# Kernel tuning notes

Hardware: AMD Instinct MI355X
Metric: run time of the kernel (lower is better)

Reference implementation:

```python
import jax, jax.numpy as jnp
import numpy as np

B, N, H, D = 1024, 128, 128, 8  # batch, num_nodes (= num variables), hidden, diffusion size


def setup_inputs() -> dict:
    key = jax.random.key(0)
    ks = jax.random.split(key, 7)
    return {
        "x": jax.random.normal(ks[0], (B, N), dtype=jnp.float32),
        "f_weight": jax.random.normal(ks[1], (N, N, H), dtype=jnp.float32) * 0.1,
        "g_weight": jax.random.normal(ks[2], (N, N, H, D), dtype=jnp.float32) * 0.1,
        "Wf": jax.random.normal(ks[3], (N, H), dtype=jnp.float32) * (1.0 / np.sqrt(H)),
        "bf": jax.random.normal(ks[4], (N,), dtype=jnp.float32) * 0.01,
        "Wg": jax.random.normal(ks[5], (N, H), dtype=jnp.float32) * (1.0 / np.sqrt(H)),
        "bg": jax.random.normal(ks[6], (N,), dtype=jnp.float32) * 0.01,
    }


def reference(x, f_weight, g_weight, Wf, bf, Wg, bg):
    # Drift f: per node i, temp_i = x @ f_weight[i]  -> [B,H]; out_i = fc_i(elu(temp_i)) -> [B,1]
    # Batched over nodes as a single einsum instead of the original Python loop.
    temp_f = jnp.einsum('bn,inh->bih', x, f_weight)              # [B,N,H]
    f_out = jnp.einsum('bih,ih->bi', jax.nn.elu(temp_f), Wf) + bf  # [B,N]

    # Diffusion g: per node i, temp_i = x @ g_weight[i] -> [B,H,D]; fc_i applied over H per diffusion channel.
    temp_g = jnp.einsum('bn,inhd->bihd', x, g_weight)            # [B,N,H,D]
    g_out = jnp.einsum('bihd,ih->bid', jax.nn.elu(temp_g), Wg) + bg[None, :, None]  # [B,N,D]
    return f_out, g_out
```

## Files before the change

kernel.cpp:

```cpp
#include <hip/hip_runtime.h>
#include <hip/hip_bf16.h>


typedef unsigned short u16;
typedef __attribute__((ext_vector_type(8))) short bf16x8;
typedef __attribute__((ext_vector_type(4))) float f32x4;

#define LOG2E 1.4426950408889634f
#define LN2   0.6931471805599453f

__device__ __forceinline__ uint32_t pk2(float a, float b) {
    union { __hip_bfloat162 h2; uint32_t u; } c;
    c.h2 = __float22bfloat162_rn(make_float2(a, b));
    return c.u;
}
__device__ __forceinline__ float elu_acc(float u, float wv, float p) {
    float m = fmaxf(u, 0.f);
    float e = __builtin_amdgcn_exp2f(fminf(u, 0.f));
    return fmaf(fmaf(m, LN2, e), wv, p);
}

__global__ __launch_bounds__(512, 2) void sde_fused(
    const float* __restrict__ x, const float* __restrict__ fw, const float* __restrict__ gw,
    const float* __restrict__ Wf, const float* __restrict__ bfp,
    const float* __restrict__ Wg, const float* __restrict__ bgp,
    float* __restrict__ out)
{
    __shared__ u16 wst[2][64 * 128];
    __shared__ float wgs[128];
    __shared__ float wfs[128];

    const int t = threadIdx.x, bx = blockIdx.x;
    const int i    = bx & 127;
    const int b0   = (bx >> 7) << 9;
    const int w    = t >> 6;
    const int lane = t & 63;
    const int l15  = lane & 15;
    const int quad = lane >> 4;
    const int l31  = lane & 31;
    const int jj   = lane >> 5;
    const int c0   = l31 * 2;
    const int sw   = (l15 >> 1) & 7;
    const int j    = w * 2 + jj;

    if (t < 128) { wgs[t] = Wg[i * 128 + t]; wfs[t] = Wf[i * 128 + t]; }

    const float* gwi = gw + (size_t)i * 131072;
    const float* fwi = fw + (size_t)i * 16384;

    float2 vr[8];
    auto load_tile = [&](int ct) {
        const float* src; int rstride;
        if (ct < 16) { src = gwi + ct * 64;        rstride = 1024; }
        else         { src = fwi + (ct - 16) * 64; rstride = 128;  }
        const float* s2 = src + (size_t)(8 * j) * rstride + c0;
        #pragma unroll
        for (int r = 0; r < 8; ++r) vr[r] = *(const float2*)(s2 + (size_t)r * rstride);
    };
    auto write_tile = [&](int p) {
        const int slot = (j ^ (l31 & 7)) << 3;
        union { uint32_t u[4]; bf16x8 v; } rr;
        rr.u[0] = pk2(vr[0].x, vr[1].x); rr.u[1] = pk2(vr[2].x, vr[3].x);
        rr.u[2] = pk2(vr[4].x, vr[5].x); rr.u[3] = pk2(vr[6].x, vr[7].x);
        *(bf16x8*)&wst[p][c0 * 128 + slot] = rr.v;
        rr.u[0] = pk2(vr[0].y, vr[1].y); rr.u[1] = pk2(vr[2].y, vr[3].y);
        rr.u[2] = pk2(vr[4].y, vr[5].y); rr.u[3] = pk2(vr[6].y, vr[7].y);
        *(bf16x8*)&wst[p][(c0 + 1) * 128 + slot] = rr.v;
    };

    load_tile(16);

    bf16x8 afr[4][4];
    #pragma unroll
    for (int rs = 0; rs < 4; ++rs) {
        const float* xr = x + (size_t)(b0 + w * 64 + rs * 16 + l15) * 128 + quad * 8;
        #pragma unroll
        for (int kk = 0; kk < 4; ++kk) {
            float4 v0 = *(const float4*)(xr + kk * 32);
            float4 v1 = *(const float4*)(xr + kk * 32 + 4);
            union { uint32_t u[4]; bf16x8 v; } r;
            r.u[0] = pk2(v0.x * LOG2E, v0.y * LOG2E);
            r.u[1] = pk2(v0.z * LOG2E, v0.w * LOG2E);
            r.u[2] = pk2(v1.x * LOG2E, v1.y * LOG2E);
            r.u[3] = pk2(v1.z * LOG2E, v1.w * LOG2E);
            afr[rs][kk] = r.v;
        }
    }

    write_tile(0);
    __syncthreads();

    float racc[16];
    #pragma unroll
    for (int q = 0; q < 16; ++q) racc[q] = 0.f;
    const float bfv = bfp[i], bgv = bgp[i];

    int p = 0;
    for (int idx = 0; idx < 18; ++idx) {
        const int ct  = (idx < 2) ? 16 + idx : idx - 2;
        const bool pre = idx < 17;
        const int ctn = (idx == 0) ? 17 : idx - 1;

        f32x4 acc[4][4];
        #pragma unroll
        for (int rs = 0; rs < 4; ++rs)
            #pragma unroll
            for (int cs = 0; cs < 4; ++cs)
                acc[rs][cs] = (f32x4){0.f, 0.f, 0.f, 0.f};

        if (pre) load_tile(ctn);

        #pragma unroll
        for (int kk = 0; kk < 4; ++kk) {
            const int co = ((kk * 4 + quad) ^ sw) << 3;
            bf16x8 bv[4];
            #pragma unroll
            for (int cs = 0; cs < 4; ++cs)
                bv[cs] = *(const bf16x8*)&wst[p][(cs * 16 + l15) * 128 + co];
            #pragma unroll
            for (int cs = 0; cs < 4; ++cs) {
                #pragma unroll
                for (int rs = 0; rs < 4; ++rs)
                    acc[rs][cs] = __builtin_amdgcn_mfma_f32_16x16x32_bf16(afr[rs][kk], bv[cs], acc[rs][cs], 0, 0, 0);
            }
        }

        if (idx < 2) {
            float wv[4];
            #pragma unroll
            for (int cs = 0; cs < 4; ++cs) wv[cs] = wfs[(ct - 16) * 64 + cs * 16 + l15];
            #pragma unroll
            for (int rs = 0; rs < 4; ++rs)
                #pragma unroll
                for (int rg = 0; rg < 4; ++rg) {
                    float s = racc[rs * 4 + rg];
                    s = elu_acc(acc[rs][0][rg], wv[0], s);
                    s = elu_acc(acc[rs][1][rg], wv[1], s);
                    s = elu_acc(acc[rs][2][rg], wv[2], s);
                    s = elu_acc(acc[rs][3][rg], wv[3], s);
                    racc[rs * 4 + rg] = s;
                }
        } else {
            float wv[4];
            #pragma unroll
            for (int cs = 0; cs < 4; ++cs) wv[cs] = wgs[ct * 8 + cs * 2 + (l15 >> 3)];
            #pragma unroll
            for (int rs = 0; rs < 4; ++rs)
                #pragma unroll
                for (int rg = 0; rg < 4; ++rg) {
                    float s = racc[rs * 4 + rg];
                    s = elu_acc(acc[rs][0][rg], wv[0], s);
                    s = elu_acc(acc[rs][1][rg], wv[1], s);
                    s = elu_acc(acc[rs][2][rg], wv[2], s);
                    s = elu_acc(acc[rs][3][rg], wv[3], s);
                    racc[rs * 4 + rg] = s;
                }
        }

        if (pre) write_tile(p ^ 1);

        if (idx == 1) {
            float Sf = 0.f;
            #pragma unroll
            for (int jh = 0; jh < 8; ++jh) Sf += wfs[jh * 16 + l15];
            #pragma unroll
            for (int rs = 0; rs < 4; ++rs)
                #pragma unroll
                for (int rg = 0; rg < 4; ++rg) {
                    float f = racc[rs * 4 + rg] - Sf;
                    f += __shfl_xor(f, 1);
                    f += __shfl_xor(f, 2);
                    f += __shfl_xor(f, 4);
                    f += __shfl_xor(f, 8);
                    if (l15 == 0) {
                        const int row = w * 64 + rs * 16 + quad * 4 + rg;
                        out[(size_t)(b0 + row) * 128 + i] = f + bfv;
                    }
                    racc[rs * 4 + rg] = 0.f;
                }
        }

        if (pre) __syncthreads();
        p ^= 1;
    }

    float Sg = 0.f;
    {
        const int hb = l15 >> 3;
        #pragma unroll 8
        for (int h = 0; h < 128; h += 2) Sg += wgs[h + hb];
    }
    #pragma unroll
    for (int rs = 0; rs < 4; ++rs)
        #pragma unroll
        for (int rg = 0; rg < 4; ++rg) {
            float g = racc[rs * 4 + rg] - Sg;
            g += __shfl_xor(g, 8);
            if (l15 < 8) {
                const int row = w * 64 + rs * 16 + quad * 4 + rg;
                out[(size_t)131072 + ((size_t)(b0 + row) * 128 + i) * 8 + (lane & 7)] = g + bgv;
            }
        }
}

extern "C" void kernel_launch(void* const* d_in, const int* in_sizes, int n_in,
                              void* d_out, int out_size, void* d_ws, size_t ws_size,
                              hipStream_t stream) {
    const float* x  = (const float*)d_in[0];
    const float* fw = (const float*)d_in[1];
    const float* gw = (const float*)d_in[2];
    const float* Wf = (const float*)d_in[3];
    const float* bf = (const float*)d_in[4];
    const float* Wg = (const float*)d_in[5];
    const float* bg = (const float*)d_in[6];
    float* out = (float*)d_out;
    (void)d_ws; (void)ws_size;

    sde_fused<<<256, 512, 0, stream>>>(x, fw, gw, Wf, bf, Wg, bg, out);
}
```

Baseline: 159.9 us.

## Software-pipeline ELU epilogue of previous tile with MFMAs of current tile

Uses two accumulator sets so that the ELU-and-weight reduction of the previous tile's MFMA results is interleaved with the MFMA issue for the current tile, per column slice. The goal is to hide the transcendental and VALU epilogue latency behind matrix-core work instead of running them back to back. In exchange it doubles the accumulator registers (64 more VGPRs), which with launch bounds of 512 threads and 2 blocks per CU may cause spills, and the f-output flush moves to step 2.

```diff
diff --git a/kernel.cpp b/kernel.cpp
--- a/kernel.cpp
+++ b/kernel.cpp
@@ -95,71 +95,52 @@
     for (int q = 0; q < 16; ++q) racc[q] = 0.f;
     const float bfv = bfp[i], bgv = bgp[i];
 
-    int p = 0;
-    for (int idx = 0; idx < 18; ++idx) {
-        const int ct  = (idx < 2) ? 16 + idx : idx - 2;
-        const bool pre = idx < 17;
-        const int ctn = (idx == 0) ? 17 : idx - 1;
-
-        f32x4 acc[4][4];
-        #pragma unroll
-        for (int rs = 0; rs < 4; ++rs)
-            #pragma unroll
-            for (int cs = 0; cs < 4; ++cs)
-                acc[rs][cs] = (f32x4){0.f, 0.f, 0.f, 0.f};
+    f32x4 accA[4][4], accB[4][4];
+
+    auto tile_step = [&](f32x4 (&cur)[4][4], f32x4 (&prv)[4][4], int idx) {
+        const bool pre     = idx < 17;
+        const int  ctn     = (idx == 0) ? 17 : idx - 1;
+        const bool hasPrev = idx > 0;
+        const int  ctp     = (idx <= 2) ? 15 + idx : idx - 3;
+        const int  p       = idx & 1;
 
         if (pre) load_tile(ctn);
 
-        #pragma unroll
-        for (int kk = 0; kk < 4; ++kk) {
-            const int co = ((kk * 4 + quad) ^ sw) << 3;
-            bf16x8 bv[4];
-            #pragma unroll
-            for (int cs = 0; cs < 4; ++cs)
-                bv[cs] = *(const bf16x8*)&wst[p][(cs * 16 + l15) * 128 + co];
-            #pragma unroll
-            for (int cs = 0; cs < 4; ++cs) {
+        float wv[4];
+        if (hasPrev) {
+            if (idx <= 2) {
+                #pragma unroll
+                for (int cs = 0; cs < 4; ++cs) wv[cs] = wfs[(ctp - 16) * 64 + cs * 16 + l15];
+            } else {
+                #pragma unroll
+                for (int cs = 0; cs < 4; ++cs) wv[cs] = wgs[ctp * 8 + cs * 2 + (l15 >> 3)];
+            }
+        }
+
+        #pragma unroll
+        for (int cs = 0; cs < 4; ++cs) {
+            #pragma unroll
+            for (int rs = 0; rs < 4; ++rs) cur[rs][cs] = (f32x4){0.f, 0.f, 0.f, 0.f};
+            #pragma unroll
+            for (int kk = 0; kk < 4; ++kk) {
+                const int co = ((kk * 4 + quad) ^ sw) << 3;
+                bf16x8 bv = *(const bf16x8*)&wst[p][(cs * 16 + l15) * 128 + co];
                 #pragma unroll
                 for (int rs = 0; rs < 4; ++rs)
-                    acc[rs][cs] = __builtin_amdgcn_mfma_f32_16x16x32_bf16(afr[rs][kk], bv[cs], acc[rs][cs], 0, 0, 0);
-            }
-        }
-
-        if (idx < 2) {
-            float wv[4];
-            #pragma unroll
-            for (int cs = 0; cs < 4; ++cs) wv[cs] = wfs[(ct - 16) * 64 + cs * 16 + l15];
-            #pragma unroll
-            for (int rs = 0; rs < 4; ++rs)
-                #pragma unroll
-                for (int rg = 0; rg < 4; ++rg) {
-                    float s = racc[rs * 4 + rg];
-                    s = elu_acc(acc[rs][0][rg], wv[0], s);
-                    s = elu_acc(acc[rs][1][rg], wv[1], s);
-                    s = elu_acc(acc[rs][2][rg], wv[2], s);
-                    s = elu_acc(acc[rs][3][rg], wv[3], s);
-                    racc[rs * 4 + rg] = s;
-                }
-        } else {
-            float wv[4];
-            #pragma unroll
-            for (int cs = 0; cs < 4; ++cs) wv[cs] = wgs[ct * 8 + cs * 2 + (l15 >> 3)];
-            #pragma unroll
-            for (int rs = 0; rs < 4; ++rs)
-                #pragma unroll
-                for (int rg = 0; rg < 4; ++rg) {
-                    float s = racc[rs * 4 + rg];
-                    s = elu_acc(acc[rs][0][rg], wv[0], s);
-                    s = elu_acc(acc[rs][1][rg], wv[1], s);
-                    s = elu_acc(acc[rs][2][rg], wv[2], s);
-                    s = elu_acc(acc[rs][3][rg], wv[3], s);
-                    racc[rs * 4 + rg] = s;
-                }
+                    cur[rs][cs] = __builtin_amdgcn_mfma_f32_16x16x32_bf16(afr[rs][kk], bv, cur[rs][cs], 0, 0, 0);
+            }
+            if (hasPrev) {
+                #pragma unroll
+                for (int rs = 0; rs < 4; ++rs)
+                    #pragma unroll
+                    for (int rg = 0; rg < 4; ++rg)
+                        racc[rs * 4 + rg] = elu_acc(prv[rs][cs][rg], wv[cs], racc[rs * 4 + rg]);
+            }
         }
 
         if (pre) write_tile(p ^ 1);
 
-        if (idx == 1) {
+        if (idx == 2) {
             float Sf = 0.f;
             #pragma unroll
             for (int jh = 0; jh < 8; ++jh) Sf += wfs[jh * 16 + l15];
@@ -181,7 +162,24 @@
         }
 
         if (pre) __syncthreads();
-        p ^= 1;
+    };
+
+    for (int it = 0; it < 9; ++it) {
+        tile_step(accA, accB, 2 * it);
+        tile_step(accB, accA, 2 * it + 1);
+    }
+
+    {
+        float wv[4];
+        #pragma unroll
+        for (int cs = 0; cs < 4; ++cs) wv[cs] = wgs[15 * 8 + cs * 2 + (l15 >> 3)];
+        #pragma unroll
+        for (int cs = 0; cs < 4; ++cs)
+            #pragma unroll
+            for (int rs = 0; rs < 4; ++rs)
+                #pragma unroll
+                for (int rg = 0; rg < 4; ++rg)
+                    racc[rs * 4 + rg] = elu_acc(accB[rs][cs][rg], wv[cs], racc[rs * 4 + rg]);
     }
 
     float Sg = 0.f;
```

Measured after the change: 173.3 us. +8.3%, slower.

## Pre-pack weights into MFMA fragment layout in workspace, drop LDS staging

Applied to the files above, without the earlier changes.

Adds a prepass kernel that converts f_weight and g_weight to bf16 and writes them in per-lane MFMA B-fragment order into the workspace. The main kernel then loads fragments straight from global memory into registers, double-buffered across tiles, with no LDS staging and no per-tile barriers. This costs an extra kernel launch and a full read-convert-write pass over the weights each call, plus heavy register pressure from two 16-fragment buffers. If the workspace is too small, it falls back to the original fused kernel.

```diff
diff --git a/kernel.cpp b/kernel.cpp
--- a/kernel.cpp
+++ b/kernel.cpp
@@ -20,13 +20,44 @@
     return fmaf(fmaf(m, LN2, e), wv, p);
 }
 
-__global__ __launch_bounds__(512, 2) void sde_fused(
-    const float* __restrict__ x, const float* __restrict__ fw, const float* __restrict__ gw,
+__global__ __launch_bounds__(256) void wt_prepass(
+    const float* __restrict__ fw, const float* __restrict__ gw, u16* __restrict__ wt)
+{
+    const int bx = blockIdx.x, t = threadIdx.x;
+    const int i    = bx / 72;
+    const int rr   = bx % 72;
+    const int sub  = t >> 6;
+    const int lane = t & 63;
+    const int l15  = lane & 15;
+    const int quad = lane >> 4;
+    const int fni  = rr * 4 + sub;
+    const int tt   = fni >> 4;
+    const int q    = fni & 15;
+    const int kk   = q >> 2;
+    const int cs   = q & 3;
+    const int c    = cs * 16 + l15;
+    const int k0   = kk * 32 + quad * 8;
+
+    const float* src; int stride;
+    if (tt < 16) { src = gw + (size_t)i * 131072 + (size_t)k0 * 1024 + tt * 64 + c;        stride = 1024; }
+    else         { src = fw + (size_t)i * 16384  + (size_t)k0 * 128  + (tt - 16) * 64 + c; stride = 128;  }
+
+    float v[8];
+    #pragma unroll
+    for (int e = 0; e < 8; ++e) v[e] = src[(size_t)e * stride];
+
+    union { uint32_t u[4]; bf16x8 w; } r;
+    r.u[0] = pk2(v[0], v[1]); r.u[1] = pk2(v[2], v[3]);
+    r.u[2] = pk2(v[4], v[5]); r.u[3] = pk2(v[6], v[7]);
+    *(bf16x8*)(wt + ((size_t)(i * 288 + fni) * 64 + lane) * 8) = r.w;
+}
+
+__global__ __launch_bounds__(512, 2) void sde_main(
+    const float* __restrict__ x, const u16* __restrict__ wt,
     const float* __restrict__ Wf, const float* __restrict__ bfp,
     const float* __restrict__ Wg, const float* __restrict__ bgp,
     float* __restrict__ out)
 {
-    __shared__ u16 wst[2][64 * 128];
     __shared__ float wgs[128];
     __shared__ float wfs[128];
 
@@ -37,38 +68,8 @@
     const int lane = t & 63;
     const int l15  = lane & 15;
     const int quad = lane >> 4;
-    const int l31  = lane & 31;
-    const int jj   = lane >> 5;
-    const int c0   = l31 * 2;
-    const int sw   = (l15 >> 1) & 7;
-    const int j    = w * 2 + jj;
 
     if (t < 128) { wgs[t] = Wg[i * 128 + t]; wfs[t] = Wf[i * 128 + t]; }
-
-    const float* gwi = gw + (size_t)i * 131072;
-    const float* fwi = fw + (size_t)i * 16384;
-
-    float2 vr[8];
-    auto load_tile = [&](int ct) {
-        const float* src; int rstride;
-        if (ct < 16) { src = gwi + ct * 64;        rstride = 1024; }
-        else         { src = fwi + (ct - 16) * 64; rstride = 128;  }
-        const float* s2 = src + (size_t)(8 * j) * rstride + c0;
-        #pragma unroll
-        for (int r = 0; r < 8; ++r) vr[r] = *(const float2*)(s2 + (size_t)r * rstride);
-    };
-    auto write_tile = [&](int p) {
-        const int slot = (j ^ (l31 & 7)) << 3;
-        union { uint32_t u[4]; bf16x8 v; } rr;
-        rr.u[0] = pk2(vr[0].x, vr[1].x); rr.u[1] = pk2(vr[2].x, vr[3].x);
-        rr.u[2] = pk2(vr[4].x, vr[5].x); rr.u[3] = pk2(vr[6].x, vr[7].x);
-        *(bf16x8*)&wst[p][c0 * 128 + slot] = rr.v;
-        rr.u[0] = pk2(vr[0].y, vr[1].y); rr.u[1] = pk2(vr[2].y, vr[3].y);
-        rr.u[2] = pk2(vr[4].y, vr[5].y); rr.u[3] = pk2(vr[6].y, vr[7].y);
-        *(bf16x8*)&wst[p][(c0 + 1) * 128 + slot] = rr.v;
-    };
-
-    load_tile(16);
 
     bf16x8 afr[4][4];
     #pragma unroll
@@ -87,19 +88,31 @@
         }
     }
 
-    write_tile(0);
     __syncthreads();
 
     float racc[16];
     #pragma unroll
-    for (int q = 0; q < 16; ++q) racc[q] = 0.f;
+    for (int qq = 0; qq < 16; ++qq) racc[qq] = 0.f;
     const float bfv = bfp[i], bgv = bgp[i];
 
-    int p = 0;
-    for (int idx = 0; idx < 18; ++idx) {
-        const int ct  = (idx < 2) ? 16 + idx : idx - 2;
-        const bool pre = idx < 17;
-        const int ctn = (idx == 0) ? 17 : idx - 1;
+    const u16* wtb = wt + (size_t)i * 288 * 512 + (size_t)lane * 8;
+
+    bf16x8 bA[16], bB[16];
+    auto load_frags = [&](bf16x8 (&bv)[16], int tt) {
+        const u16* p = wtb + (size_t)tt * 16 * 512;
+        #pragma unroll
+        for (int q = 0; q < 16; ++q) bv[q] = *(const bf16x8*)(p + q * 512);
+    };
+
+    auto compute = [&](const bf16x8 (&bv)[16], bool isF, int ct) {
+        float wv[4];
+        if (isF) {
+            #pragma unroll
+            for (int cs = 0; cs < 4; ++cs) wv[cs] = wfs[(ct - 16) * 64 + cs * 16 + l15];
+        } else {
+            #pragma unroll
+            for (int cs = 0; cs < 4; ++cs) wv[cs] = wgs[ct * 8 + cs * 2 + (l15 >> 3)];
+        }
 
         f32x4 acc[4][4];
         #pragma unroll
@@ -108,58 +121,39 @@
             for (int cs = 0; cs < 4; ++cs)
                 acc[rs][cs] = (f32x4){0.f, 0.f, 0.f, 0.f};
 
-        if (pre) load_tile(ctn);
-
-        #pragma unroll
-        for (int kk = 0; kk < 4; ++kk) {
-            const int co = ((kk * 4 + quad) ^ sw) << 3;
-            bf16x8 bv[4];
-            #pragma unroll
-            for (int cs = 0; cs < 4; ++cs)
-                bv[cs] = *(const bf16x8*)&wst[p][(cs * 16 + l15) * 128 + co];
-            #pragma unroll
-            for (int cs = 0; cs < 4; ++cs) {
+        #pragma unroll
+        for (int kk = 0; kk < 4; ++kk)
+            #pragma unroll
+            for (int cs = 0; cs < 4; ++cs)
                 #pragma unroll
                 for (int rs = 0; rs < 4; ++rs)
-                    acc[rs][cs] = __builtin_amdgcn_mfma_f32_16x16x32_bf16(afr[rs][kk], bv[cs], acc[rs][cs], 0, 0, 0);
+                    acc[rs][cs] = __builtin_amdgcn_mfma_f32_16x16x32_bf16(afr[rs][kk], bv[kk * 4 + cs], acc[rs][cs], 0, 0, 0);
+
+        #pragma unroll
+        for (int rs = 0; rs < 4; ++rs)
+            #pragma unroll
+            for (int rg = 0; rg < 4; ++rg) {
+                float s = racc[rs * 4 + rg];
+                s = elu_acc(acc[rs][0][rg], wv[0], s);
+                s = elu_acc(acc[rs][1][rg], wv[1], s);
+                s = elu_acc(acc[rs][2][rg], wv[2], s);
+                s = elu_acc(acc[rs][3][rg], wv[3], s);
+                racc[rs * 4 + rg] = s;
             }
-        }
-
-        if (idx < 2) {
-            float wv[4];
-            #pragma unroll
-            for (int cs = 0; cs < 4; ++cs) wv[cs] = wfs[(ct - 16) * 64 + cs * 16 + l15];
-            #pragma unroll
-            for (int rs = 0; rs < 4; ++rs)
-                #pragma unroll
-                for (int rg = 0; rg < 4; ++rg) {
-                    float s = racc[rs * 4 + rg];
-                    s = elu_acc(acc[rs][0][rg], wv[0], s);
-                    s = elu_acc(acc[rs][1][rg], wv[1], s);
-                    s = elu_acc(acc[rs][2][rg], wv[2], s);
-                    s = elu_acc(acc[rs][3][rg], wv[3], s);
-                    racc[rs * 4 + rg] = s;
-                }
-        } else {
-            float wv[4];
-            #pragma unroll
-            for (int cs = 0; cs < 4; ++cs) wv[cs] = wgs[ct * 8 + cs * 2 + (l15 >> 3)];
-            #pragma unroll
-            for (int rs = 0; rs < 4; ++rs)
-                #pragma unroll
-                for (int rg = 0; rg < 4; ++rg) {
-                    float s = racc[rs * 4 + rg];
-                    s = elu_acc(acc[rs][0][rg], wv[0], s);
-                    s = elu_acc(acc[rs][1][rg], wv[1], s);
-                    s = elu_acc(acc[rs][2][rg], wv[2], s);
-                    s = elu_acc(acc[rs][3][rg], wv[3], s);
-                    racc[rs * 4 + rg] = s;
-                }
-        }
-
-        if (pre) write_tile(p ^ 1);
-
-        if (idx == 1) {
+    };
+
+    load_frags(bA, 16);
+    for (int it = 0; it < 9; ++it) {
+        const int iA = 2 * it, iB = 2 * it + 1;
+        const int ttB = (iB < 2) ? 16 + iB : iB - 2;
+
+        load_frags(bB, ttB);
+        compute(bA, iA < 2, (iA < 2) ? 16 + iA : iA - 2);
+
+        if (it < 8) load_frags(bA, iA);
+        compute(bB, iB < 2, ttB);
+
+        if (it == 0) {
             float Sf = 0.f;
             #pragma unroll
             for (int jh = 0; jh < 8; ++jh) Sf += wfs[jh * 16 + l15];
@@ -179,6 +173,173 @@
                     racc[rs * 4 + rg] = 0.f;
                 }
         }
+    }
+
+    float Sg = 0.f;
+    {
+        const int hb = l15 >> 3;
+        #pragma unroll 8
+        for (int h = 0; h < 128; h += 2) Sg += wgs[h + hb];
+    }
+    #pragma unroll
+    for (int rs = 0; rs < 4; ++rs)
+        #pragma unroll
+        for (int rg = 0; rg < 4; ++rg) {
+            float g = racc[rs * 4 + rg] - Sg;
+            g += __shfl_xor(g, 8);
+            if (l15 < 8) {
+                const int row = w * 64 + rs * 16 + quad * 4 + rg;
+                out[(size_t)131072 + ((size_t)(b0 + row) * 128 + i) * 8 + (lane & 7)] = g + bgv;
+            }
+        }
+}
+
+__global__ __launch_bounds__(512, 2) void sde_fused_r7(
+    const float* __restrict__ x, const float* __restrict__ fw, const float* __restrict__ gw,
+    const float* __restrict__ Wf, const float* __restrict__ bfp,
+    const float* __restrict__ Wg, const float* __restrict__ bgp,
+    float* __restrict__ out)
+{
+    __shared__ u16 wst[2][64 * 128];
+    __shared__ float wgs[128];
+    __shared__ float wfs[128];
+
+    const int t = threadIdx.x, bx = blockIdx.x;
+    const int i    = bx & 127;
+    const int b0   = (bx >> 7) << 9;
+    const int w    = t >> 6;
+    const int lane = t & 63;
+    const int l15  = lane & 15;
+    const int quad = lane >> 4;
+    const int l31  = lane & 31;
+    const int jj   = lane >> 5;
+    const int c0   = l31 * 2;
+    const int sw   = (l15 >> 1) & 7;
+    const int j    = w * 2 + jj;
+
+    if (t < 128) { wgs[t] = Wg[i * 128 + t]; wfs[t] = Wf[i * 128 + t]; }
+
+    const float* gwi = gw + (size_t)i * 131072;
+    const float* fwi = fw + (size_t)i * 16384;
+
+    float2 vr[8];
+    auto load_tile = [&](int ct) {
+        const float* src; int rstride;
+        if (ct < 16) { src = gwi + ct * 64;        rstride = 1024; }
+        else         { src = fwi + (ct - 16) * 64; rstride = 128;  }
+        const float* s2 = src + (size_t)(8 * j) * rstride + c0;
+        #pragma unroll
+        for (int r = 0; r < 8; ++r) vr[r] = *(const float2*)(s2 + (size_t)r * rstride);
+    };
+    auto write_tile = [&](int p) {
+        const int slot = (j ^ (l31 & 7)) << 3;
+        union { uint32_t u[4]; bf16x8 v; } rr;
+        rr.u[0] = pk2(vr[0].x, vr[1].x); rr.u[1] = pk2(vr[2].x, vr[3].x);
+        rr.u[2] = pk2(vr[4].x, vr[5].x); rr.u[3] = pk2(vr[6].x, vr[7].x);
+        *(bf16x8*)&wst[p][c0 * 128 + slot] = rr.v;
+        rr.u[0] = pk2(vr[0].y, vr[1].y); rr.u[1] = pk2(vr[2].y, vr[3].y);
+        rr.u[2] = pk2(vr[4].y, vr[5].y); rr.u[3] = pk2(vr[6].y, vr[7].y);
+        *(bf16x8*)&wst[p][(c0 + 1) * 128 + slot] = rr.v;
+    };
+
+    load_tile(16);
+
+    bf16x8 afr[4][4];
+    #pragma unroll
+    for (int rs = 0; rs < 4; ++rs) {
+        const float* xr = x + (size_t)(b0 + w * 64 + rs * 16 + l15) * 128 + quad * 8;
+        #pragma unroll
+        for (int kk = 0; kk < 4; ++kk) {
+            float4 v0 = *(const float4*)(xr + kk * 32);
+            float4 v1 = *(const float4*)(xr + kk * 32 + 4);
+            union { uint32_t u[4]; bf16x8 v; } r;
+            r.u[0] = pk2(v0.x * LOG2E, v0.y * LOG2E);
+            r.u[1] = pk2(v0.z * LOG2E, v0.w * LOG2E);
+            r.u[2] = pk2(v1.x * LOG2E, v1.y * LOG2E);
+            r.u[3] = pk2(v1.z * LOG2E, v1.w * LOG2E);
+            afr[rs][kk] = r.v;
+        }
+    }
+
+    write_tile(0);
+    __syncthreads();
+
+    float racc[16];
+    #pragma unroll
+    for (int q = 0; q < 16; ++q) racc[q] = 0.f;
+    const float bfv = bfp[i], bgv = bgp[i];
+
+    int p = 0;
+    for (int idx = 0; idx < 18; ++idx) {
+        const int ct  = (idx < 2) ? 16 + idx : idx - 2;
+        const bool pre = idx < 17;
+        const int ctn = (idx == 0) ? 17 : idx - 1;
+
+        f32x4 acc[4][4];
+        #pragma unroll
+        for (int rs = 0; rs < 4; ++rs)
+            #pragma unroll
+            for (int cs = 0; cs < 4; ++cs)
+                acc[rs][cs] = (f32x4){0.f, 0.f, 0.f, 0.f};
+
+        if (pre) load_tile(ctn);
+
+        #pragma unroll
+        for (int kk = 0; kk < 4; ++kk) {
+            const int co = ((kk * 4 + quad) ^ sw) << 3;
+            bf16x8 bv[4];
+            #pragma unroll
+            for (int cs = 0; cs < 4; ++cs)
+                bv[cs] = *(const bf16x8*)&wst[p][(cs * 16 + l15) * 128 + co];
+            #pragma unroll
+            for (int cs = 0; cs < 4; ++cs)
+                #pragma unroll
+                for (int rs = 0; rs < 4; ++rs)
+                    acc[rs][cs] = __builtin_amdgcn_mfma_f32_16x16x32_bf16(afr[rs][kk], bv[cs], acc[rs][cs], 0, 0, 0);
+        }
+
+        float wv[4];
+        if (idx < 2) {
+            #pragma unroll
+            for (int cs = 0; cs < 4; ++cs) wv[cs] = wfs[(ct - 16) * 64 + cs * 16 + l15];
+        } else {
+            #pragma unroll
+            for (int cs = 0; cs < 4; ++cs) wv[cs] = wgs[ct * 8 + cs * 2 + (l15 >> 3)];
+        }
+        #pragma unroll
+        for (int rs = 0; rs < 4; ++rs)
+            #pragma unroll
+            for (int rg = 0; rg < 4; ++rg) {
+                float s = racc[rs * 4 + rg];
+                s = elu_acc(acc[rs][0][rg], wv[0], s);
+                s = elu_acc(acc[rs][1][rg], wv[1], s);
+                s = elu_acc(acc[rs][2][rg], wv[2], s);
+                s = elu_acc(acc[rs][3][rg], wv[3], s);
+                racc[rs * 4 + rg] = s;
+            }
+
+        if (pre) write_tile(p ^ 1);
+
+        if (idx == 1) {
+            float Sf = 0.f;
+            #pragma unroll
+            for (int jh = 0; jh < 8; ++jh) Sf += wfs[jh * 16 + l15];
+            #pragma unroll
+            for (int rs = 0; rs < 4; ++rs)
+                #pragma unroll
+                for (int rg = 0; rg < 4; ++rg) {
+                    float f = racc[rs * 4 + rg] - Sf;
+                    f += __shfl_xor(f, 1);
+                    f += __shfl_xor(f, 2);
+                    f += __shfl_xor(f, 4);
+                    f += __shfl_xor(f, 8);
+                    if (l15 == 0) {
+                        const int row = w * 64 + rs * 16 + quad * 4 + rg;
+                        out[(size_t)(b0 + row) * 128 + i] = f + bfv;
+                    }
+                    racc[rs * 4 + rg] = 0.f;
+                }
+        }
 
         if (pre) __syncthreads();
         p ^= 1;
@@ -214,7 +375,13 @@
     const float* Wg = (const float*)d_in[5];
     const float* bg = (const float*)d_in[6];
     float* out = (float*)d_out;
-    (void)d_ws; (void)ws_size;
-
-    sde_fused<<<256, 512, 0, stream>>>(x, fw, gw, Wf, bf, Wg, bg, out);
-}
+
+    const size_t WT_BYTES = (size_t)128 * 288 * 64 * 16;
+    if (d_ws != nullptr && ws_size >= WT_BYTES) {
+        u16* wt = (u16*)d_ws;
+        wt_prepass<<<9216, 256, 0, stream>>>(fw, gw, wt);
+        sde_main<<<256, 512, 0, stream>>>(x, wt, Wf, bf, Wg, bg, out);
+    } else {
+        sde_fused_r7<<<256, 512, 0, stream>>>(x, fw, gw, Wf, bf, Wg, bg, out);
+    }
+}
```

After: 243.5 us. 1.52x slower.
